# Kernel optimization log

Hardware: AMD Instinct MI355X
Metric: run time of the kernel (lower is better)

Reference implementation:

```python
import jax, jax.numpy as jnp
import numpy as np
import math

NUM_HEADS = 32
KV_CHANNELS = 128
LAYER_NUMBER = 4
# apply_query_key_layer_scaling=True: norm_factor = sqrt(head_dim) * layer_number,
# then scores are re-multiplied by layer_number in fp32 (numerics trick).
NORM_FACTOR = math.sqrt(KV_CHANNELS) * LAYER_NUMBER
COEFF = float(LAYER_NUMBER)
NEG = -1e9


def setup_inputs() -> dict:
    key = jax.random.key(0)
    k1, k2, k3 = jax.random.split(key, 3)
    b, h, s, d = 2, NUM_HEADS, 2048, KV_CHANNELS
    q = jax.random.normal(k1, (b, h, s, d), dtype=jnp.float32)
    k = jax.random.normal(k2, (b, h, s, d), dtype=jnp.float32)
    v = jax.random.normal(k3, (b, h, s, d), dtype=jnp.float32)
    # additive causal mask: 0 where allowed (j <= i), large negative where masked
    causal = jnp.tril(jnp.ones((s, s), dtype=bool))
    mask = jnp.where(causal, 0.0, NEG).astype(jnp.float32)[None, None, :, :]
    mask = jnp.broadcast_to(mask, (b, 1, s, s))
    return {"query_layer": q, "key_layer": k, "value_layer": v, "attention_mask": mask}


def reference(query_layer, key_layer, value_layer, attention_mask):
    b, h, sq, d = query_layer.shape
    skv = key_layer.shape[2]
    # baddbmm with beta=0, alpha=1/norm_factor  ==  (Q K^T) / norm_factor
    scores = jnp.einsum('bhqd,bhkd->bhqk', query_layer, key_layer) / NORM_FACTOR
    # attention_softmax_in_fp32 + layer scaling coefficient
    scores = scores.astype(jnp.float32) * COEFF
    scores = scores + attention_mask[:, :, :, :skv]
    probs = jax.nn.softmax(scores, axis=-1).astype(value_layer.dtype)
    # dropout p=0.0 -> identity
    context = jnp.einsum('bhqk,bhkd->bhqd', probs, value_layer)
    # transpose to [b, sq, h, d] then merge heads -> [b, sq, h*d]
    context = context.transpose(0, 2, 1, 3).reshape(b, sq, h * d)
    return context
```

## Files before the change

kernel.cpp:

```cpp
#include <hip/hip_runtime.h>
#include <cstdint>
#include <cstddef>

typedef __attribute__((ext_vector_type(8))) __bf16 bf16x8;
typedef __attribute__((ext_vector_type(4))) __bf16 bf16x4;
typedef __attribute__((ext_vector_type(4))) float f32x4;

#define SEQ 2048
#define DIM 128
#define NHEAD 32
#define NBATCH 2
#define NHEADS_TOTAL (NHEAD * NBATCH)
#define SCALE 0.08838834764831845f
#define QSC (0.08838834764831845f * 1.4426950408889634f)

#define KV_TILE 32
#define TILES_PER_HEAD (SEQ / KV_TILE)
#define TILE_ELEMS (KV_TILE * DIM)
#define K_WS_BYTES ((size_t)NHEADS_TOTAL * TILES_PER_HEAD * TILE_ELEMS * 2)
#define WS_NEEDED (2 * K_WS_BYTES)

#define PS 40

__device__ __forceinline__ float fexp2(float x) {
#if __has_builtin(__builtin_amdgcn_exp2f)
  return __builtin_amdgcn_exp2f(x);
#else
  return __expf(x * 0.69314718055994531f);
#endif
}

__global__ __launch_bounds__(256) void glm_prepass(const float* __restrict__ Kg,
                                                   const float* __restrict__ Vg,
                                                   __bf16* __restrict__ Kws,
                                                   __bf16* __restrict__ Vws) {
  __shared__ float Vl[32 * 132];
  const int hd = blockIdx.x >> 6;
  const int t  = blockIdx.x & 63;
  const int i  = threadIdx.x;
  const int kv = i >> 3, seg = i & 7;
  const size_t src   = ((size_t)hd * SEQ + (size_t)t * 32 + kv) * DIM + seg * 16;
  const size_t tbase = (size_t)(hd * TILES_PER_HEAD + t) * TILE_ELEMS;

  {
    f32x4 a = *(const f32x4*)(Kg + src);
    f32x4 b = *(const f32x4*)(Kg + src + 4);
    f32x4 c4 = *(const f32x4*)(Kg + src + 8);
    f32x4 d4 = *(const f32x4*)(Kg + src + 12);
    bf16x8 A, B;
#pragma unroll
    for (int j = 0; j < 4; ++j) {
      A[j] = (__bf16)a[j]; A[4 + j] = (__bf16)b[j];
      B[j] = (__bf16)c4[j]; B[4 + j] = (__bf16)d4[j];
    }
    const int cf = kv >> 4, lc = kv & 15, cc = seg >> 1, q0 = (seg & 1) * 2;
    const int chunkA = (cf * 4 + cc) * 64 + q0 * 16 + lc;
    *(bf16x8*)&Kws[tbase + (size_t)chunkA * 8] = A;
    *(bf16x8*)&Kws[tbase + (size_t)(chunkA + 16) * 8] = B;
  }

  {
    f32x4 a = *(const f32x4*)(Vg + src);
    f32x4 b = *(const f32x4*)(Vg + src + 4);
    f32x4 c4 = *(const f32x4*)(Vg + src + 8);
    f32x4 d4 = *(const f32x4*)(Vg + src + 12);
    float* vl = &Vl[kv * 132 + seg * 16];
    *(f32x4*)(vl + 0) = a; *(f32x4*)(vl + 4) = b;
    *(f32x4*)(vl + 8) = c4; *(f32x4*)(vl + 12) = d4;
  }
  __syncthreads();
#pragma unroll
  for (int u = 0; u < 2; ++u) {
    const int ch = i * 2 + u;
    const int nt = ch >> 6, kvg = (ch >> 4) & 3, dd = ch & 15;
    bf16x8 wv;
#pragma unroll
    for (int e = 0; e < 8; ++e) wv[e] = (__bf16)Vl[(kvg * 8 + e) * 132 + nt * 16 + dd];
    *(bf16x8*)&Vws[tbase + (size_t)ch * 8] = wv;
  }
}

__global__ __launch_bounds__(256, 2) void glm_attn_main(const float* __restrict__ Qg,
                                                        const __bf16* __restrict__ Kws,
                                                        const __bf16* __restrict__ Vws,
                                                        float* __restrict__ Out) {
  __shared__ __align__(16) __bf16 Kb[TILE_ELEMS];
  __shared__ __align__(16) __bf16 Vb[TILE_ELEMS];
  __shared__ __align__(16) __bf16 Pt[4][32 * PS];

  const int tid  = threadIdx.x;
  const int w    = tid >> 6;
  const int lane = tid & 63;
  const int quad = lane >> 4;
  const int lcol = lane & 15;

  const int qx = (int)gridDim.x - 1 - (int)blockIdx.x;
  const int qb = qx * 128;
  const int hi = blockIdx.y, bi = blockIdx.z;
  const int hd = bi * NHEAD + hi;

  const float*  Qh   = Qg + (size_t)hd * SEQ * DIM;
  const __bf16* Ksrc = Kws + (size_t)hd * TILES_PER_HEAD * TILE_ELEMS;
  const __bf16* Vsrc = Vws + (size_t)hd * TILES_PER_HEAD * TILE_ELEMS;

  bf16x8 qf[2][4];
#pragma unroll
  for (int m = 0; m < 2; ++m) {
    const float* qp = Qh + (size_t)(qb + w * 32 + m * 16 + lcol) * DIM + quad * 8;
#pragma unroll
    for (int c = 0; c < 4; ++c) {
      f32x4 a = *(const f32x4*)(qp + c * 32);
      f32x4 b = *(const f32x4*)(qp + c * 32 + 4);
      bf16x8 t;
#pragma unroll
      for (int j = 0; j < 4; ++j) {
        t[j] = (__bf16)(a[j] * QSC);
        t[4 + j] = (__bf16)(b[j] * QSC);
      }
      qf[m][c] = t;
    }
  }

  f32x4 o[2][8];
#pragma unroll
  for (int m = 0; m < 2; ++m)
#pragma unroll
    for (int n = 0; n < 8; ++n) o[m][n] = f32x4{0.f, 0.f, 0.f, 0.f};
  float lsum[2][4];
#pragma unroll
  for (int m = 0; m < 2; ++m)
#pragma unroll
    for (int r = 0; r < 4; ++r) lsum[m][r] = 0.0f;

  const int T = qx * 4 + 4;
  const int Tfull = qx * 4;

  bf16x8 kst0, kst1, vst0, vst1;
  {
    const __bf16* ks = Ksrc + (size_t)tid * 8;
    const __bf16* vs = Vsrc + (size_t)tid * 8;
    kst0 = *(const bf16x8*)ks;        kst1 = *(const bf16x8*)(ks + 2048);
    vst0 = *(const bf16x8*)vs;        vst1 = *(const bf16x8*)(vs + 2048);
  }

  for (int t = 0; t < T; ++t) {
    __syncthreads();
    *(bf16x8*)&Kb[tid * 8]        = kst0;
    *(bf16x8*)&Kb[tid * 8 + 2048] = kst1;
    *(bf16x8*)&Vb[tid * 8]        = vst0;
    *(bf16x8*)&Vb[tid * 8 + 2048] = vst1;
    __syncthreads();
    if (t + 1 < T) {
      const __bf16* ks = Ksrc + (size_t)(t + 1) * TILE_ELEMS + (size_t)tid * 8;
      const __bf16* vs = Vsrc + (size_t)(t + 1) * TILE_ELEMS + (size_t)tid * 8;
      kst0 = *(const bf16x8*)ks;      kst1 = *(const bf16x8*)(ks + 2048);
      vst0 = *(const bf16x8*)vs;      vst1 = *(const bf16x8*)(vs + 2048);
    }

    f32x4 s[2][2];
    s[0][0] = s[0][1] = s[1][0] = s[1][1] = f32x4{0.f, 0.f, 0.f, 0.f};
#pragma unroll
    for (int c = 0; c < 4; ++c) {
      bf16x8 k0 = *(const bf16x8*)&Kb[c * 512 + lane * 8];
      bf16x8 k1 = *(const bf16x8*)&Kb[(4 + c) * 512 + lane * 8];
      s[0][0] = __builtin_amdgcn_mfma_f32_16x16x32_bf16(qf[0][c], k0, s[0][0], 0, 0, 0);
      s[1][0] = __builtin_amdgcn_mfma_f32_16x16x32_bf16(qf[1][c], k0, s[1][0], 0, 0, 0);
      s[0][1] = __builtin_amdgcn_mfma_f32_16x16x32_bf16(qf[0][c], k1, s[0][1], 0, 0, 0);
      s[1][1] = __builtin_amdgcn_mfma_f32_16x16x32_bf16(qf[1][c], k1, s[1][1], 0, 0, 0);
    }

    __bf16* pw = Pt[w];
    if (t < Tfull) {
#pragma unroll
      for (int m = 0; m < 2; ++m)
#pragma unroll
        for (int cf = 0; cf < 2; ++cf)
#pragma unroll
          for (int r = 0; r < 4; ++r) {
            const float p = fexp2(fminf(s[m][cf][r], 30.0f));
            lsum[m][r] += p;
            pw[(m * 16 + quad * 4 + r) * PS + cf * 16 + lcol] = (__bf16)p;
          }
    } else {
      const int kvb = t * 32;
#pragma unroll
      for (int m = 0; m < 2; ++m) {
        const int rowb = qb + w * 32 + m * 16 + quad * 4;
#pragma unroll
        for (int cf = 0; cf < 2; ++cf) {
          const int col = kvb + cf * 16 + lcol;
#pragma unroll
          for (int r = 0; r < 4; ++r) {
            const float p = (col <= rowb + r) ? fexp2(fminf(s[m][cf][r], 30.0f)) : 0.0f;
            lsum[m][r] += p;
            pw[(m * 16 + quad * 4 + r) * PS + cf * 16 + lcol] = (__bf16)p;
          }
        }
      }
    }

    bf16x8 pf0 = *(const bf16x8*)&pw[lcol * PS + quad * 8];
    bf16x8 pf1 = *(const bf16x8*)&pw[(16 + lcol) * PS + quad * 8];
#pragma unroll
    for (int nt = 0; nt < 8; ++nt) {
      bf16x8 vf = *(const bf16x8*)&Vb[nt * 512 + lane * 8];
      o[0][nt] = __builtin_amdgcn_mfma_f32_16x16x32_bf16(pf0, vf, o[0][nt], 0, 0, 0);
      o[1][nt] = __builtin_amdgcn_mfma_f32_16x16x32_bf16(pf1, vf, o[1][nt], 0, 0, 0);
    }
  }

#pragma unroll
  for (int m = 0; m < 2; ++m)
#pragma unroll
    for (int r = 0; r < 4; ++r) {
      float v = lsum[m][r];
      v += __shfl_xor(v, 1); v += __shfl_xor(v, 2);
      v += __shfl_xor(v, 4); v += __shfl_xor(v, 8);
      lsum[m][r] = 1.0f / v;
    }
#pragma unroll
  for (int m = 0; m < 2; ++m) {
    const int row0 = qb + w * 32 + m * 16 + quad * 4;
#pragma unroll
    for (int r = 0; r < 4; ++r) {
      const float inv = lsum[m][r];
      float* op = Out + ((size_t)bi * SEQ + row0 + r) * (NHEAD * DIM) + hi * DIM + lcol;
#pragma unroll
      for (int nt = 0; nt < 8; ++nt) op[nt * 16] = o[m][nt][r] * inv;
    }
  }
}

#define KT_S 136
#define VT_S 40
#define PT_S 40

__global__ __launch_bounds__(256, 1) void glm_attn(const float* __restrict__ Qg,
                                                   const float* __restrict__ Kg,
                                                   const float* __restrict__ Vg,
                                                   float* __restrict__ Out) {
  __shared__ __align__(16) __bf16 Kt[32 * KT_S];
  __shared__ __align__(16) __bf16 Vt[128 * VT_S];
  __shared__ __align__(16) __bf16 Pa[4][16 * PT_S];

  const int tid  = threadIdx.x;
  const int wave = tid >> 6;
  const int lane = tid & 63;
  const int quad = lane >> 4;
  const int lcol = lane & 15;

  const int qbb = blockIdx.x * 64;
  const int hi = blockIdx.y;
  const int bi = blockIdx.z;

  const size_t head = ((size_t)(bi * NHEAD + hi)) * SEQ * DIM;
  const float* Qh = Qg + head;
  const float* Kh = Kg + head;
  const float* Vh = Vg + head;

  bf16x8 qf[4];
  {
    const int qrow = qbb + wave * 16 + lcol;
    const float* qp = Qh + (size_t)qrow * DIM + quad * 8;
    for (int c = 0; c < 4; ++c) {
      bf16x8 t;
      for (int j = 0; j < 8; ++j) t[j] = (__bf16)qp[c * 32 + j];
      qf[c] = t;
    }
  }

  f32x4 o[8];
  for (int n = 0; n < 8; ++n) o[n] = f32x4{0.f, 0.f, 0.f, 0.f};
  float m_r[4], l_r[4];
  for (int r = 0; r < 4; ++r) { m_r[r] = -3.0e38f; l_r[r] = 0.0f; }

  const int row0 = qbb + wave * 16 + quad * 4;
  const int ntiles = (int)blockIdx.x * 2 + 2;
  for (int t = 0; t < ntiles; ++t) {
    const int kvb = t * 32;
    __syncthreads();
    {
      const int r  = tid >> 3;
      const int c0 = (tid & 7) * 16;
      const f32x4* kp4 = (const f32x4*)(Kh + (size_t)(kvb + r) * DIM + c0);
      f32x4 ka = kp4[0], kb = kp4[1], kc = kp4[2], kd = kp4[3];
      bf16x8 lo, hi8;
      for (int j = 0; j < 4; ++j) {
        lo[j] = (__bf16)ka[j]; lo[4 + j] = (__bf16)kb[j];
        hi8[j] = (__bf16)kc[j]; hi8[4 + j] = (__bf16)kd[j];
      }
      *(bf16x8*)&Kt[r * KT_S + c0]     = lo;
      *(bf16x8*)&Kt[r * KT_S + c0 + 8] = hi8;
    }
    {
      const int kvg = (tid >> 5) * 4;
      const int dg  = (tid & 31) * 4;
      f32x4 rowv[4];
      for (int i = 0; i < 4; ++i)
        rowv[i] = *(const f32x4*)(Vh + (size_t)(kvb + kvg + i) * DIM + dg);
      for (int j = 0; j < 4; ++j) {
        bf16x4 wv;
        for (int i = 0; i < 4; ++i) wv[i] = (__bf16)rowv[i][j];
        *(bf16x4*)&Vt[(dg + j) * VT_S + kvg] = wv;
      }
    }
    __syncthreads();

    f32x4 s0 = f32x4{0.f, 0.f, 0.f, 0.f};
    f32x4 s1 = f32x4{0.f, 0.f, 0.f, 0.f};
    for (int c = 0; c < 4; ++c) {
      bf16x8 k0 = *(const bf16x8*)&Kt[lcol * KT_S + c * 32 + quad * 8];
      s0 = __builtin_amdgcn_mfma_f32_16x16x32_bf16(qf[c], k0, s0, 0, 0, 0);
      bf16x8 k1 = *(const bf16x8*)&Kt[(16 + lcol) * KT_S + c * 32 + quad * 8];
      s1 = __builtin_amdgcn_mfma_f32_16x16x32_bf16(qf[c], k1, s1, 0, 0, 0);
    }

    const int c0g = kvb + lcol;
    const int c1g = kvb + 16 + lcol;
    float p0[4], p1[4];
    for (int r = 0; r < 4; ++r) {
      const int rg = row0 + r;
      float v0 = s0[r] * SCALE;
      float v1 = s1[r] * SCALE;
      if (c0g > rg) v0 = -3.0e38f;
      if (c1g > rg) v1 = -3.0e38f;
      float tm = fmaxf(v0, v1);
      tm = fmaxf(tm, __shfl_xor(tm, 1));
      tm = fmaxf(tm, __shfl_xor(tm, 2));
      tm = fmaxf(tm, __shfl_xor(tm, 4));
      tm = fmaxf(tm, __shfl_xor(tm, 8));
      const float mn = fmaxf(m_r[r], tm);
      const float alpha = __expf(m_r[r] - mn);
      m_r[r] = mn;
      const float e0 = __expf(v0 - mn);
      const float e1 = __expf(v1 - mn);
      p0[r] = e0; p1[r] = e1;
      float rs = e0 + e1;
      rs += __shfl_xor(rs, 1);
      rs += __shfl_xor(rs, 2);
      rs += __shfl_xor(rs, 4);
      rs += __shfl_xor(rs, 8);
      l_r[r] = l_r[r] * alpha + rs;
      for (int n = 0; n < 8; ++n) o[n][r] *= alpha;
    }

    __bf16* pw = Pa[wave];
    for (int r = 0; r < 4; ++r) {
      pw[(quad * 4 + r) * PT_S + lcol]      = (__bf16)p0[r];
      pw[(quad * 4 + r) * PT_S + 16 + lcol] = (__bf16)p1[r];
    }
    bf16x8 pf = *(const bf16x8*)&pw[lcol * PT_S + quad * 8];

    for (int n = 0; n < 8; ++n) {
      bf16x8 vf = *(const bf16x8*)&Vt[(n * 16 + lcol) * VT_S + quad * 8];
      o[n] = __builtin_amdgcn_mfma_f32_16x16x32_bf16(pf, vf, o[n], 0, 0, 0);
    }
  }

  float inv_l[4];
  for (int r = 0; r < 4; ++r) inv_l[r] = 1.0f / l_r[r];
  for (int n = 0; n < 8; ++n) {
    const int col = n * 16 + lcol;
    for (int r = 0; r < 4; ++r) {
      const int row = row0 + r;
      Out[(((size_t)bi * SEQ + row) * NHEAD + hi) * DIM + col] = o[n][r] * inv_l[r];
    }
  }
}

extern "C" void kernel_launch(void* const* d_in, const int* in_sizes, int n_in,
                              void* d_out, int out_size, void* d_ws, size_t ws_size,
                              hipStream_t stream) {
  const float* Q = (const float*)d_in[0];
  const float* K = (const float*)d_in[1];
  const float* V = (const float*)d_in[2];
  float* Out = (float*)d_out;

  if (ws_size >= WS_NEEDED) {
    __bf16* Kws = (__bf16*)d_ws;
    __bf16* Vws = (__bf16*)((char*)d_ws + K_WS_BYTES);
    glm_prepass<<<dim3(NHEADS_TOTAL * TILES_PER_HEAD), 256, 0, stream>>>(K, V, Kws, Vws);
    glm_attn_main<<<dim3(SEQ / 128, NHEAD, NBATCH), 256, 0, stream>>>(Q, Kws, Vws, Out);
  } else {
    glm_attn<<<dim3(SEQ / 64, NHEAD, NBATCH), 256, 0, stream>>>(Q, K, V, Out);
  }
}
```

Before: 378.3 us.

## Fuse K/V bf16 conversion prepass into attention kernel with register prefetch

Removes the separate prepass that converted K and V to bf16 in a swizzled workspace. The attention kernel now loads fp32 K and V straight from global memory, converts and repacks them in registers into the same shared-memory layout, and prefetches the next tile into registers. This drops one kernel launch and the workspace write and re-read. In exchange, each query block re-reads and re-converts fp32 K/V, doubling the bytes loaded per tile and adding conversion work inside the main loop.

```diff
diff --git a/kernel.cpp b/kernel.cpp
--- a/kernel.cpp
+++ b/kernel.cpp
@@ -3,22 +3,14 @@
 #include <cstddef>
 
 typedef __attribute__((ext_vector_type(8))) __bf16 bf16x8;
-typedef __attribute__((ext_vector_type(4))) __bf16 bf16x4;
 typedef __attribute__((ext_vector_type(4))) float f32x4;
+typedef __attribute__((ext_vector_type(2))) float f32x2;
 
 #define SEQ 2048
 #define DIM 128
 #define NHEAD 32
 #define NBATCH 2
-#define NHEADS_TOTAL (NHEAD * NBATCH)
-#define SCALE 0.08838834764831845f
 #define QSC (0.08838834764831845f * 1.4426950408889634f)
-
-#define KV_TILE 32
-#define TILES_PER_HEAD (SEQ / KV_TILE)
-#define TILE_ELEMS (KV_TILE * DIM)
-#define K_WS_BYTES ((size_t)NHEADS_TOTAL * TILES_PER_HEAD * TILE_ELEMS * 2)
-#define WS_NEEDED (2 * K_WS_BYTES)
 
 #define PS 40
 
@@ -30,62 +22,11 @@
 #endif
 }
 
-__global__ __launch_bounds__(256) void glm_prepass(const float* __restrict__ Kg,
-                                                   const float* __restrict__ Vg,
-                                                   __bf16* __restrict__ Kws,
-                                                   __bf16* __restrict__ Vws) {
-  __shared__ float Vl[32 * 132];
-  const int hd = blockIdx.x >> 6;
-  const int t  = blockIdx.x & 63;
-  const int i  = threadIdx.x;
-  const int kv = i >> 3, seg = i & 7;
-  const size_t src   = ((size_t)hd * SEQ + (size_t)t * 32 + kv) * DIM + seg * 16;
-  const size_t tbase = (size_t)(hd * TILES_PER_HEAD + t) * TILE_ELEMS;
-
-  {
-    f32x4 a = *(const f32x4*)(Kg + src);
-    f32x4 b = *(const f32x4*)(Kg + src + 4);
-    f32x4 c4 = *(const f32x4*)(Kg + src + 8);
-    f32x4 d4 = *(const f32x4*)(Kg + src + 12);
-    bf16x8 A, B;
-#pragma unroll
-    for (int j = 0; j < 4; ++j) {
-      A[j] = (__bf16)a[j]; A[4 + j] = (__bf16)b[j];
-      B[j] = (__bf16)c4[j]; B[4 + j] = (__bf16)d4[j];
-    }
-    const int cf = kv >> 4, lc = kv & 15, cc = seg >> 1, q0 = (seg & 1) * 2;
-    const int chunkA = (cf * 4 + cc) * 64 + q0 * 16 + lc;
-    *(bf16x8*)&Kws[tbase + (size_t)chunkA * 8] = A;
-    *(bf16x8*)&Kws[tbase + (size_t)(chunkA + 16) * 8] = B;
-  }
-
-  {
-    f32x4 a = *(const f32x4*)(Vg + src);
-    f32x4 b = *(const f32x4*)(Vg + src + 4);
-    f32x4 c4 = *(const f32x4*)(Vg + src + 8);
-    f32x4 d4 = *(const f32x4*)(Vg + src + 12);
-    float* vl = &Vl[kv * 132 + seg * 16];
-    *(f32x4*)(vl + 0) = a; *(f32x4*)(vl + 4) = b;
-    *(f32x4*)(vl + 8) = c4; *(f32x4*)(vl + 12) = d4;
-  }
-  __syncthreads();
-#pragma unroll
-  for (int u = 0; u < 2; ++u) {
-    const int ch = i * 2 + u;
-    const int nt = ch >> 6, kvg = (ch >> 4) & 3, dd = ch & 15;
-    bf16x8 wv;
-#pragma unroll
-    for (int e = 0; e < 8; ++e) wv[e] = (__bf16)Vl[(kvg * 8 + e) * 132 + nt * 16 + dd];
-    *(bf16x8*)&Vws[tbase + (size_t)ch * 8] = wv;
-  }
-}
-
-__global__ __launch_bounds__(256, 2) void glm_attn_main(const float* __restrict__ Qg,
-                                                        const __bf16* __restrict__ Kws,
-                                                        const __bf16* __restrict__ Vws,
-                                                        float* __restrict__ Out) {
-  __shared__ __align__(16) __bf16 Kb[TILE_ELEMS];
-  __shared__ __align__(16) __bf16 Vb[TILE_ELEMS];
+__global__ __launch_bounds__(256, 2) void glm_attn_fused(
+    const float* __restrict__ Qg, const float* __restrict__ Kg,
+    const float* __restrict__ Vg, float* __restrict__ Out) {
+  __shared__ __align__(16) __bf16 Kb[32 * DIM];
+  __shared__ __align__(16) __bf16 Vb[32 * DIM];
   __shared__ __align__(16) __bf16 Pt[4][32 * PS];
 
   const int tid  = threadIdx.x;
@@ -99,9 +40,36 @@
   const int hi = blockIdx.y, bi = blockIdx.z;
   const int hd = bi * NHEAD + hi;
 
-  const float*  Qh   = Qg + (size_t)hd * SEQ * DIM;
-  const __bf16* Ksrc = Kws + (size_t)hd * TILES_PER_HEAD * TILE_ELEMS;
-  const __bf16* Vsrc = Vws + (size_t)hd * TILES_PER_HEAD * TILE_ELEMS;
+  const float* Qh = Qg + (size_t)hd * SEQ * DIM;
+  const float* Kh = Kg + (size_t)hd * SEQ * DIM;
+  const float* Vh = Vg + (size_t)hd * SEQ * DIM;
+
+  const float* kbase = Kh + (size_t)lcol * DIM + w * 32 + quad * 8;
+  const int vnt = tid >> 5, vkvg = (tid >> 3) & 3, vdd = (tid & 7) * 2;
+  const float* vbase = Vh + (size_t)(vkvg * 8) * DIM + vnt * 16 + vdd;
+
+  f32x4 kr0, kr1, kr2, kr3;
+  f32x2 vr0, vr1, vr2, vr3, vr4, vr5, vr6, vr7;
+
+#define PREFETCH(tt)                                                  \
+  {                                                                   \
+    const float* ka = kbase + (size_t)(tt) * (32 * DIM);              \
+    kr0 = *(const f32x4*)(ka);                                        \
+    kr1 = *(const f32x4*)(ka + 4);                                    \
+    kr2 = *(const f32x4*)(ka + 16 * DIM);                             \
+    kr3 = *(const f32x4*)(ka + 16 * DIM + 4);                         \
+    const float* va = vbase + (size_t)(tt) * (32 * DIM);              \
+    vr0 = *(const f32x2*)(va + 0 * DIM);                              \
+    vr1 = *(const f32x2*)(va + 1 * DIM);                              \
+    vr2 = *(const f32x2*)(va + 2 * DIM);                              \
+    vr3 = *(const f32x2*)(va + 3 * DIM);                              \
+    vr4 = *(const f32x2*)(va + 4 * DIM);                              \
+    vr5 = *(const f32x2*)(va + 5 * DIM);                              \
+    vr6 = *(const f32x2*)(va + 6 * DIM);                              \
+    vr7 = *(const f32x2*)(va + 7 * DIM);                              \
+  }
+
+  PREFETCH(0);
 
   bf16x8 qf[2][4];
 #pragma unroll
@@ -111,13 +79,13 @@
     for (int c = 0; c < 4; ++c) {
       f32x4 a = *(const f32x4*)(qp + c * 32);
       f32x4 b = *(const f32x4*)(qp + c * 32 + 4);
-      bf16x8 t;
+      bf16x8 tq;
 #pragma unroll
       for (int j = 0; j < 4; ++j) {
-        t[j] = (__bf16)(a[j] * QSC);
-        t[4 + j] = (__bf16)(b[j] * QSC);
+        tq[j] = (__bf16)(a[j] * QSC);
+        tq[4 + j] = (__bf16)(b[j] * QSC);
       }
-      qf[m][c] = t;
+      qf[m][c] = tq;
     }
   }
 
@@ -135,27 +103,31 @@
   const int T = qx * 4 + 4;
   const int Tfull = qx * 4;
 
-  bf16x8 kst0, kst1, vst0, vst1;
-  {
-    const __bf16* ks = Ksrc + (size_t)tid * 8;
-    const __bf16* vs = Vsrc + (size_t)tid * 8;
-    kst0 = *(const bf16x8*)ks;        kst1 = *(const bf16x8*)(ks + 2048);
-    vst0 = *(const bf16x8*)vs;        vst1 = *(const bf16x8*)(vs + 2048);
-  }
-
   for (int t = 0; t < T; ++t) {
     __syncthreads();
-    *(bf16x8*)&Kb[tid * 8]        = kst0;
-    *(bf16x8*)&Kb[tid * 8 + 2048] = kst1;
-    *(bf16x8*)&Vb[tid * 8]        = vst0;
-    *(bf16x8*)&Vb[tid * 8 + 2048] = vst1;
+    {
+      bf16x8 sA, sB;
+#pragma unroll
+      for (int j = 0; j < 4; ++j) {
+        sA[j] = (__bf16)kr0[j]; sA[4 + j] = (__bf16)kr1[j];
+        sB[j] = (__bf16)kr2[j]; sB[4 + j] = (__bf16)kr3[j];
+      }
+      *(bf16x8*)&Kb[tid * 8]        = sA;
+      *(bf16x8*)&Kb[tid * 8 + 2048] = sB;
+      bf16x8 v0, v1;
+      v0[0] = (__bf16)vr0[0]; v1[0] = (__bf16)vr0[1];
+      v0[1] = (__bf16)vr1[0]; v1[1] = (__bf16)vr1[1];
+      v0[2] = (__bf16)vr2[0]; v1[2] = (__bf16)vr2[1];
+      v0[3] = (__bf16)vr3[0]; v1[3] = (__bf16)vr3[1];
+      v0[4] = (__bf16)vr4[0]; v1[4] = (__bf16)vr4[1];
+      v0[5] = (__bf16)vr5[0]; v1[5] = (__bf16)vr5[1];
+      v0[6] = (__bf16)vr6[0]; v1[6] = (__bf16)vr6[1];
+      v0[7] = (__bf16)vr7[0]; v1[7] = (__bf16)vr7[1];
+      *(bf16x8*)&Vb[tid * 16]     = v0;
+      *(bf16x8*)&Vb[tid * 16 + 8] = v1;
+    }
     __syncthreads();
-    if (t + 1 < T) {
-      const __bf16* ks = Ksrc + (size_t)(t + 1) * TILE_ELEMS + (size_t)tid * 8;
-      const __bf16* vs = Vsrc + (size_t)(t + 1) * TILE_ELEMS + (size_t)tid * 8;
-      kst0 = *(const bf16x8*)ks;      kst1 = *(const bf16x8*)(ks + 2048);
-      vst0 = *(const bf16x8*)vs;      vst1 = *(const bf16x8*)(vs + 2048);
-    }
+    if (t + 1 < T) PREFETCH(t + 1);
 
     f32x4 s[2][2];
     s[0][0] = s[0][1] = s[1][0] = s[1][1] = f32x4{0.f, 0.f, 0.f, 0.f};
@@ -231,143 +203,6 @@
   }
 }
 
-#define KT_S 136
-#define VT_S 40
-#define PT_S 40
-
-__global__ __launch_bounds__(256, 1) void glm_attn(const float* __restrict__ Qg,
-                                                   const float* __restrict__ Kg,
-                                                   const float* __restrict__ Vg,
-                                                   float* __restrict__ Out) {
-  __shared__ __align__(16) __bf16 Kt[32 * KT_S];
-  __shared__ __align__(16) __bf16 Vt[128 * VT_S];
-  __shared__ __align__(16) __bf16 Pa[4][16 * PT_S];
-
-  const int tid  = threadIdx.x;
-  const int wave = tid >> 6;
-  const int lane = tid & 63;
-  const int quad = lane >> 4;
-  const int lcol = lane & 15;
-
-  const int qbb = blockIdx.x * 64;
-  const int hi = blockIdx.y;
-  const int bi = blockIdx.z;
-
-  const size_t head = ((size_t)(bi * NHEAD + hi)) * SEQ * DIM;
-  const float* Qh = Qg + head;
-  const float* Kh = Kg + head;
-  const float* Vh = Vg + head;
-
-  bf16x8 qf[4];
-  {
-    const int qrow = qbb + wave * 16 + lcol;
-    const float* qp = Qh + (size_t)qrow * DIM + quad * 8;
-    for (int c = 0; c < 4; ++c) {
-      bf16x8 t;
-      for (int j = 0; j < 8; ++j) t[j] = (__bf16)qp[c * 32 + j];
-      qf[c] = t;
-    }
-  }
-
-  f32x4 o[8];
-  for (int n = 0; n < 8; ++n) o[n] = f32x4{0.f, 0.f, 0.f, 0.f};
-  float m_r[4], l_r[4];
-  for (int r = 0; r < 4; ++r) { m_r[r] = -3.0e38f; l_r[r] = 0.0f; }
-
-  const int row0 = qbb + wave * 16 + quad * 4;
-  const int ntiles = (int)blockIdx.x * 2 + 2;
-  for (int t = 0; t < ntiles; ++t) {
-    const int kvb = t * 32;
-    __syncthreads();
-    {
-      const int r  = tid >> 3;
-      const int c0 = (tid & 7) * 16;
-      const f32x4* kp4 = (const f32x4*)(Kh + (size_t)(kvb + r) * DIM + c0);
-      f32x4 ka = kp4[0], kb = kp4[1], kc = kp4[2], kd = kp4[3];
-      bf16x8 lo, hi8;
-      for (int j = 0; j < 4; ++j) {
-        lo[j] = (__bf16)ka[j]; lo[4 + j] = (__bf16)kb[j];
-        hi8[j] = (__bf16)kc[j]; hi8[4 + j] = (__bf16)kd[j];
-      }
-      *(bf16x8*)&Kt[r * KT_S + c0]     = lo;
-      *(bf16x8*)&Kt[r * KT_S + c0 + 8] = hi8;
-    }
-    {
-      const int kvg = (tid >> 5) * 4;
-      const int dg  = (tid & 31) * 4;
-      f32x4 rowv[4];
-      for (int i = 0; i < 4; ++i)
-        rowv[i] = *(const f32x4*)(Vh + (size_t)(kvb + kvg + i) * DIM + dg);
-      for (int j = 0; j < 4; ++j) {
-        bf16x4 wv;
-        for (int i = 0; i < 4; ++i) wv[i] = (__bf16)rowv[i][j];
-        *(bf16x4*)&Vt[(dg + j) * VT_S + kvg] = wv;
-      }
-    }
-    __syncthreads();
-
-    f32x4 s0 = f32x4{0.f, 0.f, 0.f, 0.f};
-    f32x4 s1 = f32x4{0.f, 0.f, 0.f, 0.f};
-    for (int c = 0; c < 4; ++c) {
-      bf16x8 k0 = *(const bf16x8*)&Kt[lcol * KT_S + c * 32 + quad * 8];
-      s0 = __builtin_amdgcn_mfma_f32_16x16x32_bf16(qf[c], k0, s0, 0, 0, 0);
-      bf16x8 k1 = *(const bf16x8*)&Kt[(16 + lcol) * KT_S + c * 32 + quad * 8];
-      s1 = __builtin_amdgcn_mfma_f32_16x16x32_bf16(qf[c], k1, s1, 0, 0, 0);
-    }
-
-    const int c0g = kvb + lcol;
-    const int c1g = kvb + 16 + lcol;
-    float p0[4], p1[4];
-    for (int r = 0; r < 4; ++r) {
-      const int rg = row0 + r;
-      float v0 = s0[r] * SCALE;
-      float v1 = s1[r] * SCALE;
-      if (c0g > rg) v0 = -3.0e38f;
-      if (c1g > rg) v1 = -3.0e38f;
-      float tm = fmaxf(v0, v1);
-      tm = fmaxf(tm, __shfl_xor(tm, 1));
-      tm = fmaxf(tm, __shfl_xor(tm, 2));
-      tm = fmaxf(tm, __shfl_xor(tm, 4));
-      tm = fmaxf(tm, __shfl_xor(tm, 8));
-      const float mn = fmaxf(m_r[r], tm);
-      const float alpha = __expf(m_r[r] - mn);
-      m_r[r] = mn;
-      const float e0 = __expf(v0 - mn);
-      const float e1 = __expf(v1 - mn);
-      p0[r] = e0; p1[r] = e1;
-      float rs = e0 + e1;
-      rs += __shfl_xor(rs, 1);
-      rs += __shfl_xor(rs, 2);
-      rs += __shfl_xor(rs, 4);
-      rs += __shfl_xor(rs, 8);
-      l_r[r] = l_r[r] * alpha + rs;
-      for (int n = 0; n < 8; ++n) o[n][r] *= alpha;
-    }
-
-    __bf16* pw = Pa[wave];
-    for (int r = 0; r < 4; ++r) {
-      pw[(quad * 4 + r) * PT_S + lcol]      = (__bf16)p0[r];
-      pw[(quad * 4 + r) * PT_S + 16 + lcol] = (__bf16)p1[r];
-    }
-    bf16x8 pf = *(const bf16x8*)&pw[lcol * PT_S + quad * 8];
-
-    for (int n = 0; n < 8; ++n) {
-      bf16x8 vf = *(const bf16x8*)&Vt[(n * 16 + lcol) * VT_S + quad * 8];
-      o[n] = __builtin_amdgcn_mfma_f32_16x16x32_bf16(pf, vf, o[n], 0, 0, 0);
-    }
-  }
-
-  float inv_l[4];
-  for (int r = 0; r < 4; ++r) inv_l[r] = 1.0f / l_r[r];
-  for (int n = 0; n < 8; ++n) {
-    const int col = n * 16 + lcol;
-    for (int r = 0; r < 4; ++r) {
-      const int row = row0 + r;
-      Out[(((size_t)bi * SEQ + row) * NHEAD + hi) * DIM + col] = o[n][r] * inv_l[r];
-    }
-  }
-}
-
 extern "C" void kernel_launch(void* const* d_in, const int* in_sizes, int n_in,
                               void* d_out, int out_size, void* d_ws, size_t ws_size,
                               hipStream_t stream) {
@@ -375,13 +210,5 @@
   const float* K = (const float*)d_in[1];
   const float* V = (const float*)d_in[2];
   float* Out = (float*)d_out;
-
-  if (ws_size >= WS_NEEDED) {
-    __bf16* Kws = (__bf16*)d_ws;
-    __bf16* Vws = (__bf16*)((char*)d_ws + K_WS_BYTES);
-    glm_prepass<<<dim3(NHEADS_TOTAL * TILES_PER_HEAD), 256, 0, stream>>>(K, V, Kws, Vws);
-    glm_attn_main<<<dim3(SEQ / 128, NHEAD, NBATCH), 256, 0, stream>>>(Q, Kws, Vws, Out);
-  } else {
-    glm_attn<<<dim3(SEQ / 64, NHEAD, NBATCH), 256, 0, stream>>>(Q, K, V, Out);
-  }
+  glm_attn_fused<<<dim3(SEQ / 128, NHEAD, NBATCH), 256, 0, stream>>>(Q, K, V, Out);
 }
```

Result: slower. 388.7 us (+2.7%).
